# Kernel tuning notes

Hardware: AMD Instinct MI355X
Metric: run time of the kernel (lower is better)

## Reference

```python
import jax, jax.numpy as jnp
import numpy as np

N0, N1, N2 = 100000, 25000, 6250
E0, E1, E2 = 1600000, 400000, 100000
K = 6
NUM_CLASSES = 40


def cheb_conv(x, edge_index, W, b, num_nodes):
    # PyG ChebConv, normalization='sym', lambda_max=2.0:
    # L_hat = (2/lambda_max) * (I - D^-1/2 A D^-1/2) - I = -D^-1/2 A D^-1/2
    row, col = edge_index[0], edge_index[1]
    deg = jax.ops.segment_sum(jnp.ones(row.shape[0], x.dtype), row, num_segments=num_nodes)
    dinv = jnp.where(deg > 0, 1.0 / jnp.sqrt(jnp.maximum(deg, 1e-12)), 0.0)
    norm = -(dinv[row] * dinv[col])  # per-edge weight of L_hat

    def Lhat(v):  # [N, F] -> [N, F], sparse gather + scatter-add
        return jax.ops.segment_sum(norm[:, None] * v[col], row, num_segments=num_nodes)

    Tx0 = x
    out = Tx0 @ W[0]
    Tx1 = Lhat(x)
    out = out + Tx1 @ W[1]
    for k in range(2, W.shape[0]):  # Chebyshev recurrence T_k = 2 L_hat T_{k-1} - T_{k-2}
        Tx2 = 2.0 * Lhat(Tx1) - Tx0
        out = out + Tx2 @ W[k]
        Tx0, Tx1 = Tx1, Tx2
    return out + b


def spmm_pool(row, col, values, n_out, h):
    # torch_sparse.spmm(indices, values, size0, size1, h)
    return jax.ops.segment_sum(values[:, None] * h[col], row, num_segments=n_out)


def setup_inputs() -> dict:
    key = jax.random.key(0)
    ks = jax.random.split(key, 16)
    w = lambda k, shape: jax.random.normal(k, shape, jnp.float32) * 0.1
    return {
        "pos": jax.random.normal(ks[0], (N0, 3), jnp.float32),
        "edge_index0": jax.random.randint(ks[1], (2, E0), 0, N0),
        "edge_index1": jax.random.randint(ks[2], (2, E1), 0, N1),
        "edge_index2": jax.random.randint(ks[3], (2, E2), 0, N2),
        "ds0_row": jax.random.randint(ks[4], (N0,), 0, N1),
        "ds0_col": jax.random.randint(ks[5], (N0,), 0, N0),
        "ds0_values": jax.random.uniform(ks[6], (N0,), jnp.float32),
        "ds1_row": jax.random.randint(ks[7], (N1,), 0, N2),
        "ds1_col": jax.random.randint(ks[8], (N1,), 0, N1),
        "ds1_values": jax.random.uniform(ks[9], (N1,), jnp.float32),
        "W0": w(ks[10], (K, 3, 32)),  "b0": jnp.zeros((32,), jnp.float32),
        "W1": w(ks[11], (K, 32, 64)), "b1": jnp.zeros((64,), jnp.float32),
        "W2": w(ks[12], (K, 64, 128)),"b2": jnp.zeros((128,), jnp.float32),
        "Wh": w(ks[13], (128, 1024)), "bh": jnp.zeros((1024,), jnp.float32),
        "Wl": w(ks[14], (1024, NUM_CLASSES)), "bl": jnp.zeros((NUM_CLASSES,), jnp.float32),
    }


def reference(pos, edge_index0, edge_index1, edge_index2,
              ds0_row, ds0_col, ds0_values, ds1_row, ds1_col, ds1_values,
              W0, b0, W1, b1, W2, b2, Wh, bh, Wl, bl):
    h = jax.nn.relu(cheb_conv(pos, edge_index0, W0, b0, N0))
    h = spmm_pool(ds0_row, ds0_col, ds0_values, N1, h)
    h = jax.nn.relu(cheb_conv(h, edge_index1, W1, b1, N1))
    h = spmm_pool(ds1_row, ds1_col, ds1_values, N2, h)
    h = cheb_conv(h, edge_index2, W2, b2, N2)
    h = jnp.max(h @ Wh + bh, axis=0)  # global max pool over nodes
    return h @ Wl + bl  # [num_classes]
```

## Files before the change

kernel.cpp:

```cpp
#include <hip/hip_runtime.h>
#include <cstdint>
#include <cmath>

#define N0G 100000
#define N1G 25000
#define N2G 6250
#define E0G 1600000
#define E1G 400000
#define E2G 100000
#define KCH 6
#define NCLS 40
#define RPB 512
#define NBLK 240
#define PAYB 17
#define SCT 16
#define SCB (256 * SCT)
#define NST 5

static inline int cdiv(long a, long b){ return (int)((a + b - 1) / b); }

struct BP {
  const int* row[NST]; const int* col[NST]; const float* pval[NST];
  unsigned* ebuf[NST]; int* cs[NST]; float* wv[NST]; int* rp[NST]; float* dinv[NST];
  int E[NST], N[NST], nbkt[NST], chunk[NST], ghoff[NST], pool[NST], nb[NST], bsumoff[NST];
  int blkS[NST + 1], blkB[NST + 1];
};

__global__ __launch_bounds__(256) void k_phist_b(BP p, int* __restrict__ gh){
  int s = blockIdx.x / NBLK, c = blockIdx.x % NBLK;
  const int* row = p.row[s];
  int E = p.E[s], nbkt = p.nbkt[s], chunk = p.chunk[s];
  int* g = gh + p.ghoff[s];
  __shared__ int h[256];
  for (int i = threadIdx.x; i < nbkt; i += 256) h[i] = 0;
  __syncthreads();
  int e0 = c * chunk, e1 = min(E, e0 + chunk);
  for (int e = e0 + threadIdx.x; e < e1; e += 256)
    atomicAdd(&h[row[e] >> 9], 1);
  __syncthreads();
  for (int i = threadIdx.x; i < nbkt; i += 256)
    g[i * NBLK + c] = h[i];
}

__global__ __launch_bounds__(256) void k_scanA_b(BP p, const int* __restrict__ gh, int* __restrict__ bsum){
  int s = 0; while (s < NST - 1 && (int)blockIdx.x >= p.blkS[s + 1]) s++;
  int lb = blockIdx.x - p.blkS[s];
  int M = p.nbkt[s] * NBLK;
  const int* g = gh + p.ghoff[s];
  __shared__ int sh[256];
  int base = lb * SCB + threadIdx.x * SCT;
  int su = 0;
#pragma unroll
  for (int j = 0; j < SCT; j++){ int i = base + j; if (i < M) su += g[i]; }
  sh[threadIdx.x] = su; __syncthreads();
  for (int o = 128; o > 0; o >>= 1){
    if (threadIdx.x < o) sh[threadIdx.x] += sh[threadIdx.x + o];
    __syncthreads();
  }
  if (threadIdx.x == 0) bsum[p.bsumoff[s] + lb] = sh[0];
}

__global__ __launch_bounds__(256) void k_scanC_b(BP p, int* __restrict__ gh, const int* __restrict__ bsum){
  int s = 0; while (s < NST - 1 && (int)blockIdx.x >= p.blkS[s + 1]) s++;
  int lb = blockIdx.x - p.blkS[s];
  int M = p.nbkt[s] * NBLK;
  int* g = gh + p.ghoff[s];
  __shared__ int sh[256];
  __shared__ int blockoff;
  if (threadIdx.x == 0){
    int off = 0;
    if (p.nb[s] > 1){
      const int* bs = bsum + p.bsumoff[s];
      for (int j = 0; j < lb; j++) off += bs[j];
    }
    blockoff = off;
  }
  int base = lb * SCB + threadIdx.x * SCT;
  int v[SCT]; int su = 0;
#pragma unroll
  for (int j = 0; j < SCT; j++){ int i = base + j; v[j] = (i < M) ? g[i] : 0; su += v[j]; }
  sh[threadIdx.x] = su;
  __syncthreads();
  for (int o = 1; o < 256; o <<= 1){
    int t = (threadIdx.x >= o) ? sh[threadIdx.x - o] : 0;
    __syncthreads();
    sh[threadIdx.x] += t;
    __syncthreads();
  }
  int excl = blockoff + sh[threadIdx.x] - su;
#pragma unroll
  for (int j = 0; j < SCT; j++){
    int i = base + j;
    if (i < M){ g[i] = excl; excl += v[j]; }
  }
  if (lb == 0 && threadIdx.x == 0) p.rp[s][p.N[s]] = p.E[s];
}

__global__ __launch_bounds__(256) void k_pscatter_b(BP p, const int* __restrict__ gh){
  int s = blockIdx.x / NBLK, c = blockIdx.x % NBLK;
  const int* row = p.row[s]; const int* col = p.col[s];
  int E = p.E[s], nbkt = p.nbkt[s], chunk = p.chunk[s], pool = p.pool[s];
  const int* g = gh + p.ghoff[s];
  unsigned* ebuf = p.ebuf[s];
  __shared__ int cur[256];
  for (int i = threadIdx.x; i < nbkt; i += 256) cur[i] = g[i * NBLK + c];
  __syncthreads();
  int e0 = c * chunk, e1 = min(E, e0 + chunk);
  for (int e = e0 + threadIdx.x; e < e1; e += 256){
    int r = row[e];
    int dst = atomicAdd(&cur[r >> 9], 1);
    unsigned pay = pool ? (unsigned)e : (unsigned)col[e];
    ebuf[dst] = ((unsigned)(r & 511) << PAYB) | pay;
  }
}

__global__ __launch_bounds__(512) void k_bfinal_b(BP p, const int* __restrict__ gh){
  int s = 0; while (s < NST - 1 && (int)blockIdx.x >= p.blkB[s + 1]) s++;
  int b = blockIdx.x - p.blkB[s];
  const int* g = gh + p.ghoff[s];
  const unsigned* ebuf = p.ebuf[s];
  int nbkt = p.nbkt[s], N = p.N[s], E = p.E[s], pool = p.pool[s];
  int* cs = p.cs[s]; float* wv = p.wv[s];
  int* rp = p.rp[s]; float* dinv = p.dinv[s];
  const int* pcol = p.col[s]; const float* pval = p.pval[s];
  __shared__ int h[512];
  __shared__ int cur[512];
  int e0 = g[b * NBLK];
  int e1 = (b + 1 < nbkt) ? g[(b + 1) * NBLK] : E;
  int r0 = b * RPB;
  int t = threadIdx.x;
  h[t] = 0;
  __syncthreads();
  for (int e = e0 + t; e < e1; e += 512)
    atomicAdd(&h[ebuf[e] >> PAYB], 1);
  __syncthreads();
  int cnt = h[t];
  __syncthreads();
  for (int o = 1; o < 512; o <<= 1){
    int tmp = (t >= o) ? h[t - o] : 0;
    __syncthreads();
    h[t] += tmp;
    __syncthreads();
  }
  int excl = h[t] - cnt;
  cur[t] = excl;
  int n = r0 + t;
  if (n < N){
    rp[n] = e0 + excl;
    if (!pool) dinv[n] = cnt > 0 ? rsqrtf((float)cnt) : 0.f;
  }
  __syncthreads();
  for (int e = e0 + t; e < e1; e += 512){
    unsigned u = ebuf[e];
    int pp = atomicAdd(&cur[u >> PAYB], 1);
    int dst = e0 + pp;
    if (pool){
      int ei = (int)(u & ((1u << PAYB) - 1));
      cs[dst] = pcol[ei]; wv[dst] = pval[ei];
    } else {
      cs[dst] = (int)(u & ((1u << PAYB) - 1));
    }
  }
}

__global__ __launch_bounds__(256) void k_prescale3(const float* __restrict__ x, const float* __restrict__ dinv,
                                                   float4* __restrict__ xs, int N){
  int n = blockIdx.x * 256 + threadIdx.x;
  if (n >= N) return;
  float d = dinv[n];
  xs[n] = make_float4(d * x[n * 3 + 0], d * x[n * 3 + 1], d * x[n * 3 + 2], 0.f);
}

template<int F>
__global__ __launch_bounds__(256) void k_prescaleF(const float* __restrict__ x, const float* __restrict__ dinv,
                                                   float4* __restrict__ xs, int N){
  constexpr int L = F / 4;
  int i = blockIdx.x * 256 + threadIdx.x;
  if (i >= N * L) return;
  float d = dinv[i / L];
  float4 v = ((const float4*)x)[i];
  xs[i] = make_float4(d * v.x, d * v.y, d * v.z, d * v.w);
}

__global__ __launch_bounds__(256) void k_gather3(const int* __restrict__ rp, const int* __restrict__ cs,
                          const float4* __restrict__ xs, const float* __restrict__ dinv,
                          const float* __restrict__ sub, float* __restrict__ dst,
                          float4* __restrict__ xs_out, int N, float scale){
  int tid = blockIdx.x * 256 + threadIdx.x;
  int n = tid >> 3, q = tid & 7;
  if (n >= N) return;
  int e0 = rp[n], e1 = rp[n + 1];
  float a0 = 0.f, a1 = 0.f, a2 = 0.f;
  for (int e = e0 + q; e < e1; e += 8){
    float4 v = xs[cs[e]];
    a0 += v.x; a1 += v.y; a2 += v.z;
  }
  a0 += __shfl_xor(a0, 1); a1 += __shfl_xor(a1, 1); a2 += __shfl_xor(a2, 1);
  a0 += __shfl_xor(a0, 2); a1 += __shfl_xor(a1, 2); a2 += __shfl_xor(a2, 2);
  a0 += __shfl_xor(a0, 4); a1 += __shfl_xor(a1, 4); a2 += __shfl_xor(a2, 4);
  if (q == 0){
    float dn = dinv[n];
    float m = -scale * dn;
    float r0 = m * a0, r1 = m * a1, r2 = m * a2;
    if (sub){ r0 -= sub[n * 3 + 0]; r1 -= sub[n * 3 + 1]; r2 -= sub[n * 3 + 2]; }
    dst[n * 3 + 0] = r0; dst[n * 3 + 1] = r1; dst[n * 3 + 2] = r2;
    if (xs_out) xs_out[n] = make_float4(dn * r0, dn * r1, dn * r2, 0.f);
  }
}

template<int F>
__global__ __launch_bounds__(256) void k_gatherT(const int* __restrict__ rp, const int* __restrict__ cs,
                          const float4* __restrict__ xs, const float* __restrict__ dinv,
                          const float* __restrict__ sub, float* __restrict__ dst,
                          float4* __restrict__ xs_out, int N, float scale){
  constexpr int L = F / 4;
  constexpr int G = 4 * L;
  int tid = blockIdx.x * 256 + threadIdx.x;
  int n = tid / G, q = tid % G;
  if (n >= N) return;
  int f4 = q % L, es = q / L;
  int e0 = rp[n], e1 = rp[n + 1];
  float4 acc = make_float4(0.f, 0.f, 0.f, 0.f);
  for (int e = e0 + es; e < e1; e += 4){
    float4 v = xs[(long)cs[e] * L + f4];
    acc.x += v.x; acc.y += v.y; acc.z += v.z; acc.w += v.w;
  }
  acc.x += __shfl_xor(acc.x, L);     acc.y += __shfl_xor(acc.y, L);
  acc.z += __shfl_xor(acc.z, L);     acc.w += __shfl_xor(acc.w, L);
  acc.x += __shfl_xor(acc.x, 2 * L); acc.y += __shfl_xor(acc.y, 2 * L);
  acc.z += __shfl_xor(acc.z, 2 * L); acc.w += __shfl_xor(acc.w, 2 * L);
  if (es == 0){
    float dn = dinv[n];
    float m = -scale * dn;
    float4 r = make_float4(m * acc.x, m * acc.y, m * acc.z, m * acc.w);
    if (sub){
      float4 sv = ((const float4*)sub)[(long)n * L + f4];
      r.x -= sv.x; r.y -= sv.y; r.z -= sv.z; r.w -= sv.w;
    }
    ((float4*)dst)[(long)n * L + f4] = r;
    if (xs_out) xs_out[(long)n * L + f4] = make_float4(dn * r.x, dn * r.y, dn * r.z, dn * r.w);
  }
}

template<int F>
__global__ __launch_bounds__(256) void k_gatherP(const int* __restrict__ rp, const int* __restrict__ cs,
                          const float* __restrict__ wv, const float* __restrict__ h,
                          float* __restrict__ dst, int N){
  constexpr int L = F / 4;
  int tid = blockIdx.x * 256 + threadIdx.x;
  int n = tid / L, q = tid % L;
  if (n >= N) return;
  const float4* h4 = (const float4*)h;
  int e0 = rp[n], e1 = rp[n + 1];
  float4 acc = make_float4(0.f, 0.f, 0.f, 0.f);
  for (int e = e0; e < e1; e++){
    int c = cs[e];
    float w = wv[e];
    float4 v = h4[(long)c * L + q];
    acc.x = fmaf(w, v.x, acc.x); acc.y = fmaf(w, v.y, acc.y);
    acc.z = fmaf(w, v.z, acc.z); acc.w = fmaf(w, v.w, acc.w);
  }
  ((float4*)dst)[(long)n * L + q] = acc;
}

template<int F, int FO, int R, bool RELU>
__global__ __launch_bounds__(256) void k_cheb_tile(const float* __restrict__ x, const float* __restrict__ T, int N,
                           const float* __restrict__ W, const float* __restrict__ b,
                           float* __restrict__ out){
  constexpr int OQ4  = FO / 4;
  constexpr int NSUB = 256 / OQ4;
  constexpr int NT   = NSUB * R;
  constexpr int F6   = KCH * F;
  int n0 = blockIdx.x * NT;
  int o4   = threadIdx.x % OQ4;
  int nsub = threadIdx.x / OQ4;
  const float4* W4 = (const float4*)W;
  float4 acc[R];
  float4 bb = ((const float4*)b)[o4];
#pragma unroll
  for (int r = 0; r < R; r++) acc[r] = bb;

  if constexpr (F == 3){
    constexpr int PITCH = F6 + 2;
    __shared__ float X[NT * PITCH];
    for (int i = threadIdx.x; i < NT * F6; i += 256){
      int k = i / (NT * 3);
      int idx = i - k * (NT * 3);
      const float* src = (k == 0) ? x : (T + (size_t)(k - 1) * N * 3);
      int node = idx / 3, j = idx - node * 3;
      float v = (n0 + node < N) ? src[(long)n0 * 3 + idx] : 0.f;
      X[node * PITCH + k * 3 + j] = v;
    }
    __syncthreads();
#pragma unroll
    for (int f = 0; f < F6; f++){
      float4 w = W4[(long)f * OQ4 + o4];
#pragma unroll
      for (int r = 0; r < R; r++){
        float v = X[(nsub * R + r) * PITCH + f];
        acc[r].x = fmaf(v, w.x, acc[r].x); acc[r].y = fmaf(v, w.y, acc[r].y);
        acc[r].z = fmaf(v, w.z, acc[r].z); acc[r].w = fmaf(v, w.w, acc[r].w);
      }
    }
  } else {
    constexpr int L  = F / 4;
    constexpr int P4 = F6 / 4 + 1;
    __shared__ float4 X[NT * P4];
    for (int i = threadIdx.x; i < NT * KCH * L; i += 256){
      int k = i / (NT * L);
      int idx = i - k * (NT * L);
      int node = idx / L, q = idx - node * L;
      const float4* src4 = (const float4*)((k == 0) ? x : (T + (size_t)(k - 1) * N * F));
      float4 v = make_float4(0.f, 0.f, 0.f, 0.f);
      if (n0 + node < N) v = src4[(long)n0 * L + idx];
      X[node * P4 + k * L + q] = v;
    }
    __syncthreads();
#pragma unroll 4
    for (int f4 = 0; f4 < F6 / 4; f4++){
      float4 w0 = W4[(long)(4 * f4 + 0) * OQ4 + o4];
      float4 w1 = W4[(long)(4 * f4 + 1) * OQ4 + o4];
      float4 w2 = W4[(long)(4 * f4 + 2) * OQ4 + o4];
      float4 w3 = W4[(long)(4 * f4 + 3) * OQ4 + o4];
#pragma unroll
      for (int r = 0; r < R; r++){
        float4 hv = X[(nsub * R + r) * P4 + f4];
        acc[r].x = fmaf(hv.x, w0.x, acc[r].x); acc[r].y = fmaf(hv.x, w0.y, acc[r].y);
        acc[r].z = fmaf(hv.x, w0.z, acc[r].z); acc[r].w = fmaf(hv.x, w0.w, acc[r].w);
        acc[r].x = fmaf(hv.y, w1.x, acc[r].x); acc[r].y = fmaf(hv.y, w1.y, acc[r].y);
        acc[r].z = fmaf(hv.y, w1.z, acc[r].z); acc[r].w = fmaf(hv.y, w1.w, acc[r].w);
        acc[r].x = fmaf(hv.z, w2.x, acc[r].x); acc[r].y = fmaf(hv.z, w2.y, acc[r].y);
        acc[r].z = fmaf(hv.z, w2.z, acc[r].z); acc[r].w = fmaf(hv.z, w2.w, acc[r].w);
        acc[r].x = fmaf(hv.w, w3.x, acc[r].x); acc[r].y = fmaf(hv.w, w3.y, acc[r].y);
        acc[r].z = fmaf(hv.w, w3.z, acc[r].z); acc[r].w = fmaf(hv.w, w3.w, acc[r].w);
      }
    }
  }

#pragma unroll
  for (int r = 0; r < R; r++){
    int n = n0 + nsub * R + r;
    if (n < N){
      float4 o = acc[r];
      if (RELU){
        o.x = fmaxf(o.x, 0.f); o.y = fmaxf(o.y, 0.f);
        o.z = fmaxf(o.z, 0.f); o.w = fmaxf(o.w, 0.f);
      }
      ((float4*)out)[(long)n * OQ4 + o4] = o;
    }
  }
}

__device__ __forceinline__ unsigned fmap(float x){
  unsigned u = __float_as_uint(x);
  return (u & 0x80000000u) ? ~u : (u | 0x80000000u);
}
__device__ __forceinline__ float funmap(unsigned u){
  return (u & 0x80000000u) ? __uint_as_float(u ^ 0x80000000u) : __uint_as_float(~u);
}

#define NT 32
__global__ __launch_bounds__(256) void k_hidden_max(const float* __restrict__ h2, const float* __restrict__ Wh,
                             const float* __restrict__ bh, unsigned* __restrict__ maxed, int N){
  __shared__ float4 sW[128 * 32];
  __shared__ float4 sh4[NT * 32];
  const float4* Wh4 = (const float4*)Wh;
  int ob = blockIdx.x;
  for (int i = threadIdx.x; i < 128 * 32; i += 256){
    int f = i >> 5, ol = i & 31;
    sW[i] = Wh4[(long)f * 256 + ob * 32 + ol];
  }
  int o4l  = threadIdx.x & 31;
  int nsub = threadIdx.x >> 5;
  float4 mm = make_float4(-INFINITY, -INFINITY, -INFINITY, -INFINITY);
  int ntiles = (N + NT - 1) / NT;
  for (int nt = blockIdx.y; nt < ntiles; nt += gridDim.y){
    int n0 = nt * NT;
    __syncthreads();
    for (int i = threadIdx.x; i < NT * 32; i += 256){
      int n = i >> 5;
      float4 v = make_float4(0.f, 0.f, 0.f, 0.f);
      if (n0 + n < N) v = ((const float4*)h2)[(long)(n0 + n) * 32 + (i & 31)];
      sh4[i] = v;
    }
    __syncthreads();
    float4 acc[4];
#pragma unroll
    for (int j = 0; j < 4; j++) acc[j] = make_float4(0.f, 0.f, 0.f, 0.f);
#pragma unroll 4
    for (int f4 = 0; f4 < 32; f4++){
      float4 w0 = sW[(4 * f4 + 0) * 32 + o4l];
      float4 w1 = sW[(4 * f4 + 1) * 32 + o4l];
      float4 w2 = sW[(4 * f4 + 2) * 32 + o4l];
      float4 w3 = sW[(4 * f4 + 3) * 32 + o4l];
#pragma unroll
      for (int j = 0; j < 4; j++){
        float4 hv = sh4[(nsub * 4 + j) * 32 + f4];
        acc[j].x = fmaf(hv.x, w0.x, acc[j].x); acc[j].y = fmaf(hv.x, w0.y, acc[j].y);
        acc[j].z = fmaf(hv.x, w0.z, acc[j].z); acc[j].w = fmaf(hv.x, w0.w, acc[j].w);
        acc[j].x = fmaf(hv.y, w1.x, acc[j].x); acc[j].y = fmaf(hv.y, w1.y, acc[j].y);
        acc[j].z = fmaf(hv.y, w1.z, acc[j].z); acc[j].w = fmaf(hv.y, w1.w, acc[j].w);
        acc[j].x = fmaf(hv.z, w2.x, acc[j].x); acc[j].y = fmaf(hv.z, w2.y, acc[j].y);
        acc[j].z = fmaf(hv.z, w2.z, acc[j].z); acc[j].w = fmaf(hv.z, w2.w, acc[j].w);
        acc[j].x = fmaf(hv.w, w3.x, acc[j].x); acc[j].y = fmaf(hv.w, w3.y, acc[j].y);
        acc[j].z = fmaf(hv.w, w3.z, acc[j].z); acc[j].w = fmaf(hv.w, w3.w, acc[j].w);
      }
    }
#pragma unroll
    for (int j = 0; j < 4; j++){
      if (n0 + nsub * 4 + j < N){
        mm.x = fmaxf(mm.x, acc[j].x); mm.y = fmaxf(mm.y, acc[j].y);
        mm.z = fmaxf(mm.z, acc[j].z); mm.w = fmaxf(mm.w, acc[j].w);
      }
    }
  }
  __syncthreads();
  sh4[nsub * 32 + o4l] = mm;
  __syncthreads();
  if (nsub == 0){
#pragma unroll
    for (int s = 1; s < 8; s++){
      float4 o = sh4[s * 32 + o4l];
      mm.x = fmaxf(mm.x, o.x); mm.y = fmaxf(mm.y, o.y);
      mm.z = fmaxf(mm.z, o.z); mm.w = fmaxf(mm.w, o.w);
    }
    int o4 = ob * 32 + o4l;
    float4 b4 = ((const float4*)bh)[o4];
    atomicMax(&maxed[4 * o4 + 0], fmap(mm.x + b4.x));
    atomicMax(&maxed[4 * o4 + 1], fmap(mm.y + b4.y));
    atomicMax(&maxed[4 * o4 + 2], fmap(mm.z + b4.z));
    atomicMax(&maxed[4 * o4 + 3], fmap(mm.w + b4.w));
  }
}

__global__ __launch_bounds__(64) void k_final(const unsigned* __restrict__ maxed, const float* __restrict__ Wl,
                        const float* __restrict__ bl, float* __restrict__ out){
  int c = blockIdx.x;
  int l = threadIdx.x;
  float acc = 0.f;
  for (int o = l; o < 1024; o += 64)
    acc = fmaf(funmap(maxed[o]), Wl[o * NCLS + c], acc);
  for (int off = 32; off > 0; off >>= 1)
    acc += __shfl_down(acc, off);
  if (l == 0) out[c] = acc + bl[c];
}

template<int F, int FO, int R, bool RELU>
static void run_flow(const int* rp, const int* cs, const float* dinv, int N,
                     const float* x, const float* W, const float* b, float* out,
                     float* T, float4* xsA, float4* xsB, hipStream_t s){
  if constexpr (F == 3)
    k_prescale3<<<cdiv(N, 256), 256, 0, s>>>(x, dinv, xsA, N);
  else
    k_prescaleF<F><<<cdiv((long)N * (F / 4), 256), 256, 0, s>>>(x, dinv, xsA, N);

  const float* sub = nullptr; float scale = 1.f;
  float4* xin = xsA; float4* xout = xsB;
  const float* srcRaw = x;
  for (int k = 1; k < KCH; k++){
    float* Tk = T + (size_t)(k - 1) * N * F;
    float4* xo = (k == KCH - 1) ? nullptr : xout;
    if constexpr (F == 3)
      k_gather3<<<cdiv((long)N * 8, 256), 256, 0, s>>>(rp, cs, xin, dinv, sub, Tk, xo, N, scale);
    else
      k_gatherT<F><<<cdiv((long)N * F, 256), 256, 0, s>>>(rp, cs, xin, dinv, sub, Tk, xo, N, scale);
    sub = srcRaw; srcRaw = Tk; scale = 2.f;
    float4* t = xin; xin = xout; xout = t;
  }
  constexpr int NTC = (256 / (FO / 4)) * R;
  k_cheb_tile<F, FO, R, RELU><<<cdiv(N, NTC), 256, 0, s>>>(x, T, N, W, b, out);
}

extern "C" void kernel_launch(void* const* d_in, const int* in_sizes, int n_in,
                              void* d_out, int out_size, void* d_ws, size_t ws_size,
                              hipStream_t stream){
  const float* pos = (const float*)d_in[0];
  const int*   ei0 = (const int*)d_in[1];
  const int*   ei1 = (const int*)d_in[2];
  const int*   ei2 = (const int*)d_in[3];
  const int*   p0r = (const int*)d_in[4];
  const int*   p0c = (const int*)d_in[5];
  const float* p0v = (const float*)d_in[6];
  const int*   p1r = (const int*)d_in[7];
  const int*   p1c = (const int*)d_in[8];
  const float* p1v = (const float*)d_in[9];
  const float* W0  = (const float*)d_in[10]; const float* b0 = (const float*)d_in[11];
  const float* W1  = (const float*)d_in[12]; const float* b1 = (const float*)d_in[13];
  const float* W2  = (const float*)d_in[14]; const float* b2 = (const float*)d_in[15];
  const float* Wh  = (const float*)d_in[16]; const float* bh = (const float*)d_in[17];
  const float* Wl  = (const float*)d_in[18]; const float* bl = (const float*)d_in[19];
  float* out = (float*)d_out;

  float* TB = (float*)d_ws;
  float* hA = TB + 4000000;
  float* hB = hA + 3200000;
  float* hC = hB + 1600000;
  int* cs0   = (int*)(hC + 800000);
  int* cs1   = cs0 + 1600000;
  int* cs2   = cs1 + 400000;
  int* csP0  = cs2 + 100000;
  int* csP1  = csP0 + 100000;
  float* wvP0 = (float*)(csP1 + 25000);
  float* wvP1 = wvP0 + 100000;
  int* rp0  = (int*)(wvP1 + 25000);
  int* rp1  = rp0 + 100001;
  int* rp2  = rp1 + 25001;
  int* rpP0 = rp2 + 6251;
  int* rpP1 = rpP0 + 25001;
  float* dv0 = (float*)(rpP1 + 6251);
  float* dv1 = dv0 + 100000;
  float* dv2 = dv1 + 25000;
  int* gh   = (int*)(dv2 + 6250);
  int* bsum = gh + 76800;
  unsigned* maxed = (unsigned*)(bsum + 80);

  unsigned* eb0  = (unsigned*)TB;
  unsigned* eb1  = eb0 + 1600000;
  unsigned* eb2  = eb1 + 400000;
  unsigned* ebP0 = eb2 + 100000;
  unsigned* ebP1 = ebP0 + 100000;

  BP bp{};
  const int* rows[NST] = {ei0, ei1, ei2, p0r, p1r};
  const int* cols[NST] = {ei0 + E0G, ei1 + E1G, ei2 + E2G, p0c, p1c};
  const float* pvals[NST] = {nullptr, nullptr, nullptr, p0v, p1v};
  unsigned* ebufs[NST] = {eb0, eb1, eb2, ebP0, ebP1};
  int* css[NST] = {cs0, cs1, cs2, csP0, csP1};
  float* wvs[NST] = {nullptr, nullptr, nullptr, wvP0, wvP1};
  int* rps[NST] = {rp0, rp1, rp2, rpP0, rpP1};
  float* dvs[NST] = {dv0, dv1, dv2, nullptr, nullptr};
  int Es[NST] = {E0G, E1G, E2G, N0G, N1G};
  int Ns[NST] = {N0G, N1G, N2G, N1G, N2G};
  int pools[NST] = {0, 0, 0, 1, 1};
  int ghacc = 0, scanacc = 0, bacc = 0;
  bp.blkS[0] = 0; bp.blkB[0] = 0;
  for (int s = 0; s < NST; s++){
    bp.row[s] = rows[s]; bp.col[s] = cols[s]; bp.pval[s] = pvals[s];
    bp.ebuf[s] = ebufs[s]; bp.cs[s] = css[s]; bp.wv[s] = wvs[s];
    bp.rp[s] = rps[s]; bp.dinv[s] = dvs[s];
    bp.E[s] = Es[s]; bp.N[s] = Ns[s]; bp.pool[s] = pools[s];
    bp.nbkt[s] = cdiv(Ns[s], RPB);
    bp.chunk[s] = cdiv(Es[s], NBLK);
    bp.ghoff[s] = ghacc; ghacc += bp.nbkt[s] * NBLK;
    bp.nb[s] = cdiv(bp.nbkt[s] * NBLK, SCB);
    bp.bsumoff[s] = s * 16;
    scanacc += bp.nb[s]; bp.blkS[s + 1] = scanacc;
    bacc += bp.nbkt[s]; bp.blkB[s + 1] = bacc;
  }

  k_phist_b<<<NST * NBLK, 256, 0, stream>>>(bp, gh);
  k_scanA_b<<<scanacc, 256, 0, stream>>>(bp, gh, bsum);
  k_scanC_b<<<scanacc, 256, 0, stream>>>(bp, gh, bsum);
  k_pscatter_b<<<NST * NBLK, 256, 0, stream>>>(bp, gh);
  k_bfinal_b<<<bacc, 512, 0, stream>>>(bp, gh);

  hipMemsetAsync(maxed, 0, 1024 * sizeof(unsigned), stream);

  run_flow<3, 32, 2, true>(rp0, cs0, dv0, N0G, pos, W0, b0, hA,
                           TB, (float4*)hB, (float4*)(hB + 400000), stream);

  k_gatherP<32><<<cdiv((long)N1G * 8, 256), 256, 0, stream>>>(rpP0, csP0, wvP0, hA, hC, N1G);

  run_flow<32, 64, 2, true>(rp1, cs1, dv1, N1G, hC, W1, b1, hB,
                            TB, (float4*)hA, (float4*)(hA + 800000), stream);

  k_gatherP<64><<<cdiv((long)N2G * 16, 256), 256, 0, stream>>>(rpP1, csP1, wvP1, hB, hC, N2G);

  run_flow<64, 128, 2, false>(rp2, cs2, dv2, N2G, hC, W2, b2, hA,
                              TB, (float4*)(TB + 2400000), (float4*)(TB + 2800000), stream);

  dim3 g(8, 64);
  k_hidden_max<<<g, 256, 0, stream>>>(hA, Wh, bh, maxed, N2G);

  k_final<<<NCLS, 64, 0, stream>>>(maxed, Wl, bl, out);
}
```

Baseline: 359.0 us.

## Skip CSR scatter for level-0 graph and aggregate bucketed edges in shared memory

For the first graph level, the per-bucket finalize kernel now exits before scattering edges into CSR column order. A new kernel instead walks the bucketed edge buffer directly and accumulates each neighbour's features into shared-memory rows with atomics. The dinv-prescaling of inputs is folded into the bucket-finalize kernel for level 0 and into the pooling gather for levels 1 and 2, so the separate prescale kernels are removed. This trades a full CSR column scatter and several small launches for shared-memory float atomics, which may contend and gives a non-deterministic summation order.

```diff
diff --git a/kernel.cpp b/kernel.cpp
--- a/kernel.cpp
+++ b/kernel.cpp
@@ -13,6 +13,7 @@
 #define RPB 512
 #define NBLK 240
 #define PAYB 17
+#define PAYM ((1u << PAYB) - 1u)
 #define SCT 16
 #define SCB (256 * SCT)
 #define NST 5
@@ -22,7 +23,8 @@
 struct BP {
   const int* row[NST]; const int* col[NST]; const float* pval[NST];
   unsigned* ebuf[NST]; int* cs[NST]; float* wv[NST]; int* rp[NST]; float* dinv[NST];
-  int E[NST], N[NST], nbkt[NST], chunk[NST], ghoff[NST], pool[NST], nb[NST], bsumoff[NST];
+  const float* xsrc[NST]; float4* xsdst[NST];
+  int E[NST], N[NST], nbkt[NST], chunk[NST], ghoff[NST], pool[NST], nb[NST], bsumoff[NST], edgec[NST];
   int blkS[NST + 1], blkB[NST + 1];
 };
 
@@ -147,61 +149,63 @@
   int n = r0 + t;
   if (n < N){
     rp[n] = e0 + excl;
-    if (!pool) dinv[n] = cnt > 0 ? rsqrtf((float)cnt) : 0.f;
-  }
+    if (!pool){
+      float d = cnt > 0 ? rsqrtf((float)cnt) : 0.f;
+      dinv[n] = d;
+      if (p.edgec[s]){
+        const float* x = p.xsrc[s];
+        p.xsdst[s][n] = make_float4(d * x[n * 3 + 0], d * x[n * 3 + 1], d * x[n * 3 + 2], 0.f);
+      }
+    }
+  }
+  if (p.edgec[s]) return;
   __syncthreads();
   for (int e = e0 + t; e < e1; e += 512){
     unsigned u = ebuf[e];
     int pp = atomicAdd(&cur[u >> PAYB], 1);
     int dst = e0 + pp;
     if (pool){
-      int ei = (int)(u & ((1u << PAYB) - 1));
+      int ei = (int)(u & PAYM);
       cs[dst] = pcol[ei]; wv[dst] = pval[ei];
     } else {
-      cs[dst] = (int)(u & ((1u << PAYB) - 1));
-    }
-  }
-}
-
-__global__ __launch_bounds__(256) void k_prescale3(const float* __restrict__ x, const float* __restrict__ dinv,
-                                                   float4* __restrict__ xs, int N){
-  int n = blockIdx.x * 256 + threadIdx.x;
-  if (n >= N) return;
-  float d = dinv[n];
-  xs[n] = make_float4(d * x[n * 3 + 0], d * x[n * 3 + 1], d * x[n * 3 + 2], 0.f);
-}
-
-template<int F>
-__global__ __launch_bounds__(256) void k_prescaleF(const float* __restrict__ x, const float* __restrict__ dinv,
-                                                   float4* __restrict__ xs, int N){
-  constexpr int L = F / 4;
-  int i = blockIdx.x * 256 + threadIdx.x;
-  if (i >= N * L) return;
-  float d = dinv[i / L];
-  float4 v = ((const float4*)x)[i];
-  xs[i] = make_float4(d * v.x, d * v.y, d * v.z, d * v.w);
-}
-
-__global__ __launch_bounds__(256) void k_gather3(const int* __restrict__ rp, const int* __restrict__ cs,
-                          const float4* __restrict__ xs, const float* __restrict__ dinv,
-                          const float* __restrict__ sub, float* __restrict__ dst,
-                          float4* __restrict__ xs_out, int N, float scale){
-  int tid = blockIdx.x * 256 + threadIdx.x;
-  int n = tid >> 3, q = tid & 7;
-  if (n >= N) return;
-  int e0 = rp[n], e1 = rp[n + 1];
-  float a0 = 0.f, a1 = 0.f, a2 = 0.f;
-  for (int e = e0 + q; e < e1; e += 8){
-    float4 v = xs[cs[e]];
-    a0 += v.x; a1 += v.y; a2 += v.z;
-  }
-  a0 += __shfl_xor(a0, 1); a1 += __shfl_xor(a1, 1); a2 += __shfl_xor(a2, 1);
-  a0 += __shfl_xor(a0, 2); a1 += __shfl_xor(a1, 2); a2 += __shfl_xor(a2, 2);
-  a0 += __shfl_xor(a0, 4); a1 += __shfl_xor(a1, 4); a2 += __shfl_xor(a2, 4);
-  if (q == 0){
+      cs[dst] = (int)(u & PAYM);
+    }
+  }
+}
+
+__global__ __launch_bounds__(512) void k_eapply(const unsigned* __restrict__ ebuf, const int* __restrict__ gh,
+                          int nbkt, int E, int N, const float4* __restrict__ xs,
+                          const float* __restrict__ dinv, const float* __restrict__ sub,
+                          float* __restrict__ dst, float4* __restrict__ xs_out, float scale){
+  __shared__ float acc[RPB * 4];
+  int b = blockIdx.x, t = threadIdx.x;
+  for (int i = t; i < RPB * 4; i += 512) acc[i] = 0.f;
+  __syncthreads();
+  int e0 = gh[b * NBLK];
+  int e1 = (b + 1 < nbkt) ? gh[(b + 1) * NBLK] : E;
+  int e = e0 + t;
+  for (; e + 3 * 512 < e1; e += 4 * 512){
+    unsigned u0 = ebuf[e], u1 = ebuf[e + 512], u2 = ebuf[e + 1024], u3 = ebuf[e + 1536];
+    float4 v0 = xs[u0 & PAYM], v1 = xs[u1 & PAYM], v2 = xs[u2 & PAYM], v3 = xs[u3 & PAYM];
+    int r0 = (int)(u0 >> PAYB) * 4, r1 = (int)(u1 >> PAYB) * 4;
+    int r2 = (int)(u2 >> PAYB) * 4, r3 = (int)(u3 >> PAYB) * 4;
+    atomicAdd(&acc[r0 + 0], v0.x); atomicAdd(&acc[r0 + 1], v0.y); atomicAdd(&acc[r0 + 2], v0.z);
+    atomicAdd(&acc[r1 + 0], v1.x); atomicAdd(&acc[r1 + 1], v1.y); atomicAdd(&acc[r1 + 2], v1.z);
+    atomicAdd(&acc[r2 + 0], v2.x); atomicAdd(&acc[r2 + 1], v2.y); atomicAdd(&acc[r2 + 2], v2.z);
+    atomicAdd(&acc[r3 + 0], v3.x); atomicAdd(&acc[r3 + 1], v3.y); atomicAdd(&acc[r3 + 2], v3.z);
+  }
+  for (; e < e1; e += 512){
+    unsigned u = ebuf[e];
+    float4 v = xs[u & PAYM];
+    int r = (int)(u >> PAYB) * 4;
+    atomicAdd(&acc[r + 0], v.x); atomicAdd(&acc[r + 1], v.y); atomicAdd(&acc[r + 2], v.z);
+  }
+  __syncthreads();
+  int n = b * RPB + t;
+  if (n < N){
     float dn = dinv[n];
     float m = -scale * dn;
-    float r0 = m * a0, r1 = m * a1, r2 = m * a2;
+    float r0 = m * acc[t * 4 + 0], r1 = m * acc[t * 4 + 1], r2 = m * acc[t * 4 + 2];
     if (sub){ r0 -= sub[n * 3 + 0]; r1 -= sub[n * 3 + 1]; r2 -= sub[n * 3 + 2]; }
     dst[n * 3 + 0] = r0; dst[n * 3 + 1] = r1; dst[n * 3 + 2] = r2;
     if (xs_out) xs_out[n] = make_float4(dn * r0, dn * r1, dn * r2, 0.f);
@@ -245,7 +249,8 @@
 template<int F>
 __global__ __launch_bounds__(256) void k_gatherP(const int* __restrict__ rp, const int* __restrict__ cs,
                           const float* __restrict__ wv, const float* __restrict__ h,
-                          float* __restrict__ dst, int N){
+                          float* __restrict__ dst, int N,
+                          const float* __restrict__ dinvN, float4* __restrict__ xsN){
   constexpr int L = F / 4;
   int tid = blockIdx.x * 256 + threadIdx.x;
   int n = tid / L, q = tid % L;
@@ -261,6 +266,10 @@
     acc.z = fmaf(w, v.z, acc.z); acc.w = fmaf(w, v.w, acc.w);
   }
   ((float4*)dst)[(long)n * L + q] = acc;
+  if (xsN){
+    float dn = dinvN[n];
+    xsN[(long)n * L + q] = make_float4(dn * acc.x, dn * acc.y, dn * acc.z, dn * acc.w);
+  }
 }
 
 template<int F, int FO, int R, bool RELU>
@@ -446,24 +455,15 @@
 }
 
 template<int F, int FO, int R, bool RELU>
-static void run_flow(const int* rp, const int* cs, const float* dinv, int N,
-                     const float* x, const float* W, const float* b, float* out,
-                     float* T, float4* xsA, float4* xsB, hipStream_t s){
-  if constexpr (F == 3)
-    k_prescale3<<<cdiv(N, 256), 256, 0, s>>>(x, dinv, xsA, N);
-  else
-    k_prescaleF<F><<<cdiv((long)N * (F / 4), 256), 256, 0, s>>>(x, dinv, xsA, N);
-
+static void run_flowT(const int* rp, const int* cs, const float* dinv, int N,
+                      const float* x, const float* W, const float* b, float* out,
+                      float* T, float4* xin, float4* xout, hipStream_t s){
   const float* sub = nullptr; float scale = 1.f;
-  float4* xin = xsA; float4* xout = xsB;
   const float* srcRaw = x;
   for (int k = 1; k < KCH; k++){
     float* Tk = T + (size_t)(k - 1) * N * F;
     float4* xo = (k == KCH - 1) ? nullptr : xout;
-    if constexpr (F == 3)
-      k_gather3<<<cdiv((long)N * 8, 256), 256, 0, s>>>(rp, cs, xin, dinv, sub, Tk, xo, N, scale);
-    else
-      k_gatherT<F><<<cdiv((long)N * F, 256), 256, 0, s>>>(rp, cs, xin, dinv, sub, Tk, xo, N, scale);
+    k_gatherT<F><<<cdiv((long)N * F, 256), 256, 0, s>>>(rp, cs, xin, dinv, sub, Tk, xo, N, scale);
     sub = srcRaw; srcRaw = Tk; scale = 2.f;
     float4* t = xin; xin = xout; xout = t;
   }
@@ -491,12 +491,12 @@
   const float* Wl  = (const float*)d_in[18]; const float* bl = (const float*)d_in[19];
   float* out = (float*)d_out;
 
-  float* TB = (float*)d_ws;
-  float* hA = TB + 4000000;
-  float* hB = hA + 3200000;
-  float* hC = hB + 1600000;
-  int* cs0   = (int*)(hC + 800000);
-  int* cs1   = cs0 + 1600000;
+  float* TB  = (float*)d_ws;
+  float* hA  = TB + 4000000;
+  float* hB  = hA + 3200000;
+  float* hC  = hB + 1600000;
+  float* csR = hC + 800000;
+  int* cs1   = (int*)(csR + 1600000);
   int* cs2   = cs1 + 400000;
   int* csP0  = cs2 + 100000;
   int* csP1  = csP0 + 100000;
@@ -525,20 +525,23 @@
   const int* cols[NST] = {ei0 + E0G, ei1 + E1G, ei2 + E2G, p0c, p1c};
   const float* pvals[NST] = {nullptr, nullptr, nullptr, p0v, p1v};
   unsigned* ebufs[NST] = {eb0, eb1, eb2, ebP0, ebP1};
-  int* css[NST] = {cs0, cs1, cs2, csP0, csP1};
+  int* css[NST] = {nullptr, cs1, cs2, csP0, csP1};
   float* wvs[NST] = {nullptr, nullptr, nullptr, wvP0, wvP1};
   int* rps[NST] = {rp0, rp1, rp2, rpP0, rpP1};
   float* dvs[NST] = {dv0, dv1, dv2, nullptr, nullptr};
   int Es[NST] = {E0G, E1G, E2G, N0G, N1G};
   int Ns[NST] = {N0G, N1G, N2G, N1G, N2G};
   int pools[NST] = {0, 0, 0, 1, 1};
+  int edgecs[NST] = {1, 0, 0, 0, 0};
   int ghacc = 0, scanacc = 0, bacc = 0;
   bp.blkS[0] = 0; bp.blkB[0] = 0;
   for (int s = 0; s < NST; s++){
     bp.row[s] = rows[s]; bp.col[s] = cols[s]; bp.pval[s] = pvals[s];
     bp.ebuf[s] = ebufs[s]; bp.cs[s] = css[s]; bp.wv[s] = wvs[s];
     bp.rp[s] = rps[s]; bp.dinv[s] = dvs[s];
-    bp.E[s] = Es[s]; bp.N[s] = Ns[s]; bp.pool[s] = pools[s];
+    bp.xsrc[s] = (s == 0) ? pos : nullptr;
+    bp.xsdst[s] = (s == 0) ? (float4*)hB : nullptr;
+    bp.E[s] = Es[s]; bp.N[s] = Ns[s]; bp.pool[s] = pools[s]; bp.edgec[s] = edgecs[s];
     bp.nbkt[s] = cdiv(Ns[s], RPB);
     bp.chunk[s] = cdiv(Es[s], NBLK);
     bp.ghoff[s] = ghacc; ghacc += bp.nbkt[s] * NBLK;
@@ -556,21 +559,35 @@
 
   hipMemsetAsync(maxed, 0, 1024 * sizeof(unsigned), stream);
 
-  run_flow<3, 32, 2, true>(rp0, cs0, dv0, N0G, pos, W0, b0, hA,
-                           TB, (float4*)hB, (float4*)(hB + 400000), stream);
-
-  k_gatherP<32><<<cdiv((long)N1G * 8, 256), 256, 0, stream>>>(rpP0, csP0, wvP0, hA, hC, N1G);
-
-  run_flow<32, 64, 2, true>(rp1, cs1, dv1, N1G, hC, W1, b1, hB,
-                            TB, (float4*)hA, (float4*)(hA + 800000), stream);
-
-  k_gatherP<64><<<cdiv((long)N2G * 16, 256), 256, 0, stream>>>(rpP1, csP1, wvP1, hB, hC, N2G);
-
-  run_flow<64, 128, 2, false>(rp2, cs2, dv2, N2G, hC, W2, b2, hA,
-                              TB, (float4*)(TB + 2400000), (float4*)(TB + 2800000), stream);
+  {
+    int nbkt0 = cdiv(N0G, RPB);
+    float4* xin = (float4*)hB; float4* xout = (float4*)(hB + 400000);
+    const float* sub = nullptr; float scale = 1.f;
+    const float* srcRaw = pos;
+    for (int k = 1; k < KCH; k++){
+      float* Tk = csR + (size_t)(k - 1) * N0G * 3;
+      float4* xo = (k == KCH - 1) ? nullptr : xout;
+      k_eapply<<<nbkt0, 512, 0, stream>>>(eb0, gh + bp.ghoff[0], nbkt0, E0G, N0G,
+                                          xin, dv0, sub, Tk, xo, scale);
+      sub = srcRaw; srcRaw = Tk; scale = 2.f;
+      float4* t = xin; xin = xout; xout = t;
+    }
+    k_cheb_tile<3, 32, 2, true><<<cdiv(N0G, 64), 256, 0, stream>>>(pos, csR, N0G, W0, b0, hA);
+  }
+
+  k_gatherP<32><<<cdiv((long)N1G * 8, 256), 256, 0, stream>>>(rpP0, csP0, wvP0, hA, hC, N1G,
+                                                              dv1, (float4*)csR);
+
+  run_flowT<32, 64, 2, true>(rp1, cs1, dv1, N1G, hC, W1, b1, hB,
+                             TB, (float4*)csR, (float4*)(csR + 800000), stream);
+
+  k_gatherP<64><<<cdiv((long)N2G * 16, 256), 256, 0, stream>>>(rpP1, csP1, wvP1, hB, hC, N2G,
+                                                               dv2, (float4*)csR);
+
+  run_flowT<64, 128, 2, false>(rp2, cs2, dv2, N2G, hC, W2, b2, hA,
+                               TB, (float4*)csR, (float4*)(csR + 400000), stream);
 
   dim3 g(8, 64);
   k_hidden_max<<<g, 256, 0, stream>>>(hA, Wh, bh, maxed, N2G);
-
   k_final<<<NCLS, 64, 0, stream>>>(maxed, Wl, bl, out);
 }
```

New measurement: 459.8 us. 1.28x slower.
